# Kernel tuning notes

Measured on AMD Instinct MI355X. Metric: run time of the kernel, lower is better.

The kernel has to match this reference:

```python
import jax, jax.numpy as jnp
import numpy as np

D_MODEL = 1024
N_HEADS = 16
D_K = D_MODEL // N_HEADS
D_FF = 4 * D_MODEL
MEM = 32
EPS = 1e-6
NEG = -1e9


def layer_norm(x, alpha, bias):
    # torch: alpha * (x - mean) / (std_unbiased + eps) + bias
    mean = jnp.mean(x, axis=-1, keepdims=True)
    std = jnp.sqrt(jnp.var(x, axis=-1, keepdims=True, ddof=1))
    return alpha * (x - mean) / (std + EPS) + bias


def setup_inputs() -> dict:
    key = jax.random.key(0)
    ks = jax.random.split(key, 12)
    B, S = 4, 2048
    s = 1.0 / np.sqrt(D_MODEL)
    inp = {
        "x": jax.random.normal(ks[0], (B, S, D_MODEL), jnp.float32),
        "mask": jnp.ones((1, 1, S, S + MEM), jnp.int32),
        "memory_tokens": jax.random.normal(ks[1], (MEM, D_MODEL), jnp.float32),
        "w_q": jax.random.normal(ks[2], (D_MODEL, D_MODEL), jnp.float32) * s,
        "w_k": jax.random.normal(ks[3], (D_MODEL, D_MODEL), jnp.float32) * s,
        "w_v": jax.random.normal(ks[4], (D_MODEL, D_MODEL), jnp.float32) * s,
        "w_o": jax.random.normal(ks[5], (D_MODEL, D_MODEL), jnp.float32) * s,
        "ln1_alpha": jnp.ones((D_MODEL,), jnp.float32),
        "ln1_bias": jnp.zeros((D_MODEL,), jnp.float32),
        "ln2_alpha": jnp.ones((D_MODEL,), jnp.float32),
        "ln2_bias": jnp.zeros((D_MODEL,), jnp.float32),
        "ff_w1": jax.random.normal(ks[6], (D_MODEL, D_FF), jnp.float32) * s,
        "ff_b1": jnp.zeros((D_FF,), jnp.float32),
        "ff_w2": jax.random.normal(ks[7], (D_FF, D_MODEL), jnp.float32) * (1.0 / np.sqrt(D_FF)),
        "ff_b2": jnp.zeros((D_MODEL,), jnp.float32),
    }
    return inp


def reference(x, mask, memory_tokens, w_q, w_k, w_v, w_o,
              ln1_alpha, ln1_bias, ln2_alpha, ln2_bias,
              ff_w1, ff_b1, ff_w2, ff_b2):
    B, S, D = x.shape
    memory = jnp.broadcast_to(memory_tokens[None], (B, MEM, D))

    # --- residual 1: self attention with memory K/V ---
    xn = layer_norm(x, ln1_alpha, ln1_bias)
    q = (xn @ w_q).reshape(B, S, N_HEADS, D_K).transpose(0, 2, 1, 3)  # [B,h,S,dk]
    k = (xn @ w_k).reshape(B, S, N_HEADS, D_K).transpose(0, 2, 1, 3)
    v = (xn @ w_v).reshape(B, S, N_HEADS, D_K).transpose(0, 2, 1, 3)
    mem_k = (memory @ w_k).reshape(B, MEM, N_HEADS, D_K).transpose(0, 2, 1, 3)
    mem_v = (memory @ w_v).reshape(B, MEM, N_HEADS, D_K).transpose(0, 2, 1, 3)
    k = jnp.concatenate([mem_k, k], axis=2)  # [B,h,M+S,dk]
    v = jnp.concatenate([mem_v, v], axis=2)

    scores = jnp.einsum("bhsd,bhtd->bhst", q, k) / np.sqrt(D_K)  # [B,h,S,M+S]
    scores = jnp.where(mask == 0, NEG, scores)
    attn = jax.nn.softmax(scores, axis=-1)
    ctx = jnp.einsum("bhst,bhtd->bhsd", attn, v)
    ctx = ctx.transpose(0, 2, 1, 3).reshape(B, S, D)
    x = x + ctx @ w_o

    # --- residual 2: FFN ---
    xn2 = layer_norm(x, ln2_alpha, ln2_bias)
    ff = jax.nn.relu(xn2 @ ff_w1 + ff_b1) @ ff_w2 + ff_b2
    x = x + ff

    new_memory = jnp.broadcast_to(jnp.mean(x, axis=1, keepdims=True), (B, MEM, D))
    return (x, new_memory)
```

## Files before the change

### kernel.cpp

```cpp
#include <hip/hip_runtime.h>
#include <hip/hip_bf16.h>
#include <cstdint>
#include <cstddef>


typedef __attribute__((ext_vector_type(8))) short short8;
typedef __attribute__((ext_vector_type(4))) float floatx4;
typedef __attribute__((ext_vector_type(4))) unsigned short ushort4v;

#define NB   4
#define SEQ  2048
#define DM   1024
#define DKH  64
#define TT   2080
#define DFF  4096
#define NMEM 32

static __device__ __forceinline__ float bu2f(unsigned short u) {
  return __uint_as_float(((unsigned int)u) << 16);
}
static __device__ __forceinline__ unsigned short f2bu(float x) {
  __hip_bfloat16 h = __float2bfloat16(x);
  return *reinterpret_cast<unsigned short*>(&h);
}
static __device__ __forceinline__ float fast_exp2(float x) {
#if __has_builtin(__builtin_amdgcn_exp2f)
  return __builtin_amdgcn_exp2f(x);
#else
  return exp2f(x);
#endif
}
static __device__ __forceinline__ void async16(const void* g, void* l) {
  __builtin_amdgcn_global_load_lds(
      (const __attribute__((address_space(1))) void*)g,
      (__attribute__((address_space(3))) void*)l, 16, 0, 0);
}

#define PREP_X   8192
#define PREP_MT  (PREP_X + 32)
#define PREP_SM  (PREP_MT + 9)
#define PREP_T   (PREP_SM + 3072)

__global__ __launch_bounds__(256) void prep(
    const void* __restrict__ x,   const void* __restrict__ memtok,
    const void* __restrict__ wq,  const void* __restrict__ wk,
    const void* __restrict__ wv,  const void* __restrict__ wo,
    const void* __restrict__ fw1, const void* __restrict__ fw2,
    const void* __restrict__ ln1a, const void* __restrict__ ln1b,
    const void* __restrict__ ln2a, const void* __restrict__ ln2b,
    const void* __restrict__ fb1, const void* __restrict__ fb2,
    unsigned short* __restrict__ xb, unsigned short* __restrict__ MT,
    unsigned short* __restrict__ Wtq, unsigned short* __restrict__ Wtk,
    unsigned short* __restrict__ Wtv, unsigned short* __restrict__ Wto,
    unsigned short* __restrict__ Wt1, unsigned short* __restrict__ Wt2,
    unsigned short* __restrict__ L1A, unsigned short* __restrict__ L1B,
    unsigned short* __restrict__ L2A, unsigned short* __restrict__ L2B,
    unsigned short* __restrict__ FB1, unsigned short* __restrict__ FB2,
    int* __restrict__ FLAG)
{
  const int tid = threadIdx.x;
  const unsigned short probe = ((const unsigned short*)x)[tid & 63];
  const unsigned e = (probe >> 7) & 0xFF;
  const bool ok = (e == 0) || (e >= 100 && e <= 141);
  const int flag = (__ballot(!ok) != 0ULL) ? 1 : 0;
  const int bid = blockIdx.x;
  if (bid == 0 && tid == 0) *FLAG = flag;

  if (bid < PREP_T && bid >= PREP_SM) {
    const int tb = bid - PREP_SM;
    const void* in; unsigned short* outp; int R, C, tx, ty;
    if (tb < 1024) {
      const int w = tb >> 8, lt = tb & 255;
      in = (w == 0) ? wq : (w == 1) ? wk : (w == 2) ? wv : wo;
      outp = (w == 0) ? Wtq : (w == 1) ? Wtk : (w == 2) ? Wtv : Wto;
      R = DM; C = DM; tx = lt & 15; ty = lt >> 4;
    } else if (tb < 2048) {
      const int lt = tb - 1024;
      in = fw1; outp = Wt1; R = DM; C = DFF; tx = lt & 63; ty = lt >> 6;
    } else {
      const int lt = tb - 2048;
      in = fw2; outp = Wt2; R = DFF; C = DM; tx = lt & 15; ty = lt >> 4;
    }
    __shared__ unsigned short tile[64][65];
    const int r0 = ty << 6, c0 = tx << 6;
    const int lr = tid >> 2, lc = (tid & 3) << 4;
    if (flag) {
      const float* ip = (const float*)in + (size_t)(r0 + lr) * C + c0 + lc;
#pragma unroll
      for (int q = 0; q < 16; q += 4) {
        floatx4 f = *(const floatx4*)(ip + q);
        tile[lr][lc+q+0] = f2bu(f[0]); tile[lr][lc+q+1] = f2bu(f[1]);
        tile[lr][lc+q+2] = f2bu(f[2]); tile[lr][lc+q+3] = f2bu(f[3]);
      }
    } else {
      const unsigned short* ip = (const unsigned short*)in + (size_t)(r0 + lr) * C + c0 + lc;
#pragma unroll
      for (int q = 0; q < 16; q += 4) {
        ushort4v a = *(const ushort4v*)(ip + q);
        tile[lr][lc+q+0] = a.x; tile[lr][lc+q+1] = a.y;
        tile[lr][lc+q+2] = a.z; tile[lr][lc+q+3] = a.w;
      }
    }
    __syncthreads();
    unsigned short* op = outp + (size_t)(c0 + lr) * R + r0 + lc;
#pragma unroll
    for (int q = 0; q < 16; q += 4) {
      ushort4v a;
      a.x = tile[lc+q+0][lr]; a.y = tile[lc+q+1][lr];
      a.z = tile[lc+q+2][lr]; a.w = tile[lc+q+3][lr];
      *(ushort4v*)(op + q) = a;
    }
    return;
  }

  const void* src; unsigned short* dst; int base;
  if (bid < PREP_X)      { src = x;      dst = xb; base = bid * 1024; }
  else if (bid < PREP_MT){ src = memtok; dst = MT; base = (bid - PREP_X) * 1024; }
  else {
    const int s = bid - PREP_MT; base = 0;
    if      (s == 0) { src = ln1a; dst = L1A; }
    else if (s == 1) { src = ln1b; dst = L1B; }
    else if (s == 2) { src = ln2a; dst = L2A; }
    else if (s == 3) { src = ln2b; dst = L2B; }
    else if (s <= 7) { src = fb1;  dst = FB1; base = (s - 4) * 1024; }
    else             { src = fb2;  dst = FB2; }
  }
  const int i = base + tid * 4;
  if (flag) {
    const float* s4 = (const float*)src + i;
    ushort4v o;
    o.x = f2bu(s4[0]); o.y = f2bu(s4[1]); o.z = f2bu(s4[2]); o.w = f2bu(s4[3]);
    *(ushort4v*)&dst[i] = o;
  } else {
    *(ushort4v*)&dst[i] = *(const ushort4v*)&((const unsigned short*)src)[i];
  }
}

__global__ __launch_bounds__(512, 2) void gemm256(
    const unsigned short* __restrict__ A, int lda,
    const unsigned short* __restrict__ Bt, int ldbt,
    const unsigned short* __restrict__ bias,
    const unsigned short* __restrict__ resid_b,
    const float* __restrict__ resid_f,
    void* __restrict__ outp, void* __restrict__ outp2, void* __restrict__ outp3,
    int M, int N, int K, int relu, int mode, const int* __restrict__ dt)
{
  __shared__ __align__(16) unsigned short As[2][256 * 64];
  __shared__ __align__(16) unsigned short Bs[2][256 * 64];

  const int tid  = threadIdx.x;
  const int lane = tid & 63;
  const int wv   = tid >> 6;
  const int quad = lane >> 4;
  const int lr   = lane & 15;
  const int wr   = wv >> 2;
  const int wc   = wv & 3;
  const int arow = wr * 128;
  const int bcol = wc * 64;

  const int gx  = gridDim.x;
  const int nwg = gx * gridDim.y;
  int wg = blockIdx.y * gx + blockIdx.x;
  { const int q = nwg >> 3, rI = nwg & 7, xc = wg & 7, ix = wg >> 3;
    wg = (xc < rI ? xc * (q + 1) : rI * (q + 1) + (xc - rI) * q) + ix; }
  const int by = wg / gx;
  const int bx = wg - by * gx;
  const int m0 = by * 256;
  const int n0 = bx * 256;

  floatx4 acc[8][4];
#pragma unroll
  for (int i = 0; i < 8; ++i)
#pragma unroll
    for (int j = 0; j < 4; ++j) { floatx4 z = {0.f, 0.f, 0.f, 0.f}; acc[i][j] = z; }

  auto stage = [&](int buf, int kk) {
#pragma unroll
    for (int j = 0; j < 4; ++j) {
      const int g   = j * 512 + tid;
      const int row = g >> 3;
      const int kc  = (g & 7) ^ (row & 7);
      int gr = m0 + row; gr = gr < M ? gr : (M - 1);
      async16(A  + (size_t)gr * lda + kk + kc * 8,
              &As[buf][(size_t)(j * 512 + (tid & ~63)) * 8]);
      const int gn = n0 + row;
      async16(Bt + (size_t)gn * ldbt + kk + kc * 8,
              &Bs[buf][(size_t)(j * 512 + (tid & ~63)) * 8]);
    }
  };

  const int nk = K >> 6;
  stage(0, 0);
  int cur = 0;
  for (int it = 0; it < nk; ++it) {
    if (it + 1 < nk) {
      stage(cur ^ 1, (it + 1) << 6);
      asm volatile("s_waitcnt vmcnt(8)" ::: "memory");
    } else {
      asm volatile("s_waitcnt vmcnt(0)" ::: "memory");
    }
    __builtin_amdgcn_s_barrier();

    const unsigned short* Ab = &As[cur][0];
    const unsigned short* Bb = &Bs[cur][0];
#pragma unroll
    for (int ks = 0; ks < 2; ++ks) {
      short8 bfr[4], af[4];
#pragma unroll
      for (int ni = 0; ni < 4; ++ni) {
        const int row = bcol + ni * 16 + lr;
        bfr[ni] = *(const short8*)&Bb[row * 64 + (((ks * 4 + quad) ^ (lr & 7)) * 8)];
      }
#pragma unroll
      for (int mi = 0; mi < 4; ++mi) {
        const int row = arow + mi * 16 + lr;
        af[mi] = *(const short8*)&Ab[row * 64 + (((ks * 4 + quad) ^ (lr & 7)) * 8)];
      }
      __builtin_amdgcn_s_setprio(1);
#pragma unroll
      for (int mi = 0; mi < 4; ++mi)
#pragma unroll
        for (int ni = 0; ni < 4; ++ni)
          acc[mi][ni] = __builtin_amdgcn_mfma_f32_16x16x32_bf16(af[mi], bfr[ni], acc[mi][ni], 0, 0, 0);
      __builtin_amdgcn_s_setprio(0);
      __builtin_amdgcn_sched_barrier(0);
#pragma unroll
      for (int mi = 0; mi < 4; ++mi) {
        const int row = arow + 64 + mi * 16 + lr;
        af[mi] = *(const short8*)&Ab[row * 64 + (((ks * 4 + quad) ^ (lr & 7)) * 8)];
      }
      __builtin_amdgcn_s_setprio(1);
#pragma unroll
      for (int mi = 0; mi < 4; ++mi)
#pragma unroll
        for (int ni = 0; ni < 4; ++ni)
          acc[4 + mi][ni] = __builtin_amdgcn_mfma_f32_16x16x32_bf16(af[mi], bfr[ni], acc[4 + mi][ni], 0, 0, 0);
      __builtin_amdgcn_s_setprio(0);
      __builtin_amdgcn_sched_barrier(0);
    }

    asm volatile("s_waitcnt lgkmcnt(0)" ::: "memory");
    __builtin_amdgcn_s_barrier();
    cur ^= 1;
  }

  if (mode == 5) {
    const int cbase  = n0 + bcol;
    const int sector = cbase >> 10;
    const int clb    = cbase & 1023;
    unsigned short* Qo = (unsigned short*)outp;
    unsigned short* Ko = (unsigned short*)outp2;
    unsigned short* Vo = (unsigned short*)outp3;
#pragma unroll
    for (int mi = 0; mi < 8; ++mi) {
      const int rb = m0 + arow + mi * 16 + quad * 4;
#pragma unroll
      for (int ni = 0; ni < 4; ++ni) {
        const int col = clb + ni * 16 + lr;
        if (sector == 0) {
#pragma unroll
          for (int rg = 0; rg < 4; ++rg) {
            const int r = rb + rg;
            if (r < NB * SEQ) Qo[(size_t)r * DM + col] = f2bu(acc[mi][ni][rg]);
          }
        } else if (sector == 1) {
#pragma unroll
          for (int rg = 0; rg < 4; ++rg) {
            const int r = rb + rg;
            if (r >= M) continue;
            const int row2 = (r < NB * SEQ) ? ((r >> 11) * TT + NMEM + (r & (SEQ - 1)))
                                            : (r - NB * SEQ);
            Ko[(size_t)row2 * DM + col] = f2bu(acc[mi][ni][rg]);
          }
        } else {
          if (rb < M) {
            int bb, t;
            if (rb < NB * SEQ) { bb = rb >> 11; t = NMEM + (rb & (SEQ - 1)); }
            else               { bb = 0;        t = rb - NB * SEQ; }
            ushort4v pk;
            pk.x = f2bu(acc[mi][ni][0]); pk.y = f2bu(acc[mi][ni][1]);
            pk.z = f2bu(acc[mi][ni][2]); pk.w = f2bu(acc[mi][ni][3]);
            *(ushort4v*)(Vo + ((size_t)bb * DM + col) * TT + t) = pk;
          }
        }
      }
    }
    return;
  }

  const int ofp32 = (mode == 4 && dt) ? *dt : 0;
#pragma unroll
  for (int mi = 0; mi < 8; ++mi) {
    const int rb = m0 + arow + mi * 16 + quad * 4;
#pragma unroll
    for (int ni = 0; ni < 4; ++ni) {
      const int col = n0 + bcol + ni * 16 + lr;
      const float bv = bias ? bu2f(bias[col]) : 0.0f;
#pragma unroll
      for (int rg = 0; rg < 4; ++rg) {
        const int r = rb + rg;
        if (r >= M) continue;
        float v = acc[mi][ni][rg] + bv;
        if (relu) v = fmaxf(v, 0.0f);
        if (resid_b) v += bu2f(resid_b[(size_t)r * N + col]);
        if (resid_f) v += resid_f[(size_t)r * N + col];
        const size_t idx = (size_t)r * N + col;
        if (mode == 3)       ((float*)outp)[idx] = v;
        else if (mode == 4) {
          if (ofp32) ((float*)outp)[idx] = v;
          else       ((unsigned short*)outp)[idx] = f2bu(v);
        } else               ((unsigned short*)outp)[idx] = f2bu(v);
      }
    }
  }
}

#define PSTR 72

__global__ __launch_bounds__(256, 3) void flash_attn(
    const unsigned short* __restrict__ Q,
    const unsigned short* __restrict__ Kb,
    const unsigned short* __restrict__ Vtb,
    unsigned short* __restrict__ ctx)
{
  __shared__ __align__(16) unsigned short Ks[2][64 * 64];
  __shared__ __align__(16) unsigned short Vs[2][64 * 64];
  __shared__ __align__(16) unsigned short Ps[128 * PSTR];

  const int tid  = threadIdx.x;
  const int wave = tid >> 6;
  const int lane = tid & 63;
  const int quad = lane >> 4;
  const int lr   = lane & 15;

  const int i    = blockIdx.x;
  const int pair = (i & 7) * 8 + (i >> 7);
  const int q0   = ((i >> 3) & 15) * 128;
  const int b    = pair >> 4;
  const int h    = pair & 15;

  const unsigned short* Qb  = Q   + ((size_t)(b * SEQ + q0)) * DM + h * DKH;
  const unsigned short* Kbp = Kb  + ((size_t)b * TT) * DM + h * DKH;
  const unsigned short* Vbp = Vtb + ((size_t)(b * DM + h * DKH)) * TT;

  short8 aq[2][2];
#pragma unroll
  for (int mi = 0; mi < 2; ++mi)
#pragma unroll
    for (int ks = 0; ks < 2; ++ks)
      aq[mi][ks] = *(const short8*)(Qb + (size_t)(wave * 32 + mi * 16 + lr) * DM
                                       + ks * 32 + quad * 8);

  const int srl = lane >> 3;
  const int swc = (lane & 7) ^ srl;

  floatx4 O[2][4], Osum[2];
#pragma unroll
  for (int mi = 0; mi < 2; ++mi) {
    floatx4 z = {0.f, 0.f, 0.f, 0.f};
    Osum[mi] = z;
#pragma unroll
    for (int ni = 0; ni < 4; ++ni) O[mi][ni] = z;
  }
  short8 ones;
#pragma unroll
  for (int i2 = 0; i2 < 8; ++i2) ones[i2] = (short)0x3F80;

  const float SC = 0.125f * 1.4426950408889634f;

  auto stageKV = [&](int buf, int t0s) {
#pragma unroll
    for (int i2 = 0; i2 < 2; ++i2) {
      const int rr = (wave * 2 + i2) * 8 + srl;
      int tg = t0s + rr; tg = tg < TT ? tg : (TT - 1);
      async16(Kbp + (size_t)tg * DM + swc * 8, &Ks[buf][(wave * 2 + i2) * 512]);
      int ts = t0s + swc * 8; ts = ts <= (TT - 8) ? ts : (TT - 8);
      async16(Vbp + (size_t)rr * TT + ts, &Vs[buf][(wave * 2 + i2) * 512]);
    }
  };

  stageKV(0, 0);
  int cur = 0;

  for (int t0 = 0; t0 < TT; t0 += 64) {
    if (t0 + 64 < TT) {
      stageKV(cur ^ 1, t0 + 64);
      asm volatile("s_waitcnt vmcnt(4)" ::: "memory");
    } else {
      asm volatile("s_waitcnt vmcnt(0)" ::: "memory");
    }
    __builtin_amdgcn_s_barrier();

    floatx4 sc4[2][4];
#pragma unroll
    for (int mi = 0; mi < 2; ++mi)
#pragma unroll
      for (int ni = 0; ni < 4; ++ni) { floatx4 z = {0.f, 0.f, 0.f, 0.f}; sc4[mi][ni] = z; }
#pragma unroll
    for (int ks = 0; ks < 2; ++ks) {
      short8 bk[4];
#pragma unroll
      for (int ni = 0; ni < 4; ++ni) {
        const int row = ni * 16 + lr;
        bk[ni] = *(const short8*)&Ks[cur][row * 64 + (((ks * 4 + quad) ^ (row & 7)) * 8)];
      }
      __builtin_amdgcn_s_setprio(1);
#pragma unroll
      for (int mi = 0; mi < 2; ++mi)
#pragma unroll
        for (int ni = 0; ni < 4; ++ni)
          sc4[mi][ni] = __builtin_amdgcn_mfma_f32_16x16x32_bf16(aq[mi][ks], bk[ni], sc4[mi][ni], 0, 0, 0);
      __builtin_amdgcn_s_setprio(0);
    }

    bool valid[4];
#pragma unroll
    for (int ni = 0; ni < 4; ++ni) valid[ni] = (t0 + ni * 16 + lr) < TT;

#pragma unroll
    for (int mi = 0; mi < 2; ++mi)
#pragma unroll
      for (int rg = 0; rg < 4; ++rg) {
        const int prow = wave * 32 + mi * 16 + quad * 4 + rg;
#pragma unroll
        for (int ni = 0; ni < 4; ++ni) {
          const float p = valid[ni] ? fast_exp2(sc4[mi][ni][rg] * SC) : 0.0f;
          Ps[prow * PSTR + ni * 16 + lr] =
              (unsigned short)((__float_as_uint(p) + 0x8000u) >> 16);
        }
      }

    __asm__ __volatile__("" ::: "memory");

#pragma unroll
    for (int ks = 0; ks < 2; ++ks) {
      short8 ap[2], bv[4];
#pragma unroll
      for (int mi = 0; mi < 2; ++mi)
        ap[mi] = *(const short8*)&Ps[(wave * 32 + mi * 16 + lr) * PSTR + ks * 32 + quad * 8];
#pragma unroll
      for (int ni = 0; ni < 4; ++ni) {
        const int row = ni * 16 + lr;
        bv[ni] = *(const short8*)&Vs[cur][row * 64 + (((ks * 4 + quad) ^ (row & 7)) * 8)];
      }
      __builtin_amdgcn_s_setprio(1);
#pragma unroll
      for (int mi = 0; mi < 2; ++mi) {
        Osum[mi] = __builtin_amdgcn_mfma_f32_16x16x32_bf16(ap[mi], ones, Osum[mi], 0, 0, 0);
#pragma unroll
        for (int ni = 0; ni < 4; ++ni)
          O[mi][ni] = __builtin_amdgcn_mfma_f32_16x16x32_bf16(ap[mi], bv[ni], O[mi][ni], 0, 0, 0);
      }
      __builtin_amdgcn_s_setprio(0);
    }

    asm volatile("s_waitcnt lgkmcnt(0)" ::: "memory");
    __builtin_amdgcn_s_barrier();
    cur ^= 1;
  }

#pragma unroll
  for (int mi = 0; mi < 2; ++mi)
#pragma unroll
    for (int rg = 0; rg < 4; ++rg) {
      const float inv = 1.0f / Osum[mi][rg];
      const int row = q0 + wave * 32 + mi * 16 + quad * 4 + rg;
#pragma unroll
      for (int ni = 0; ni < 4; ++ni) {
        const int col = h * DKH + ni * 16 + lr;
        ctx[((size_t)(b * SEQ + row)) * DM + col] = f2bu(O[mi][ni][rg] * inv);
      }
    }
}

__global__ __launch_bounds__(256) void ln_kernel(
    const unsigned short* __restrict__ xin_bf,
    const float* __restrict__ xin_f,
    const unsigned short* __restrict__ memtok,
    const unsigned short* __restrict__ gam,
    const unsigned short* __restrict__ bet,
    unsigned short* __restrict__ outp,
    int rows_main)
{
  const int row = blockIdx.x;
  const int tid = threadIdx.x;
  const int c0  = tid * 4;
  if (row >= rows_main) {
    const int mr = row - rows_main;
    *(ushort4v*)&outp[(size_t)row * DM + c0] =
        *(const ushort4v*)&memtok[(size_t)mr * DM + c0];
    return;
  }
  float v[4];
  if (xin_bf) {
    ushort4v u = *(const ushort4v*)&xin_bf[(size_t)row * DM + c0];
    v[0] = bu2f(u.x); v[1] = bu2f(u.y); v[2] = bu2f(u.z); v[3] = bu2f(u.w);
  } else {
    floatx4 f = *(const floatx4*)&xin_f[(size_t)row * DM + c0];
    v[0] = f[0]; v[1] = f[1]; v[2] = f[2]; v[3] = f[3];
  }
  float s  = v[0] + v[1] + v[2] + v[3];
  float ss = v[0]*v[0] + v[1]*v[1] + v[2]*v[2] + v[3]*v[3];
#pragma unroll
  for (int m = 1; m <= 32; m <<= 1) {
    s  += __shfl_xor(s, m, 64);
    ss += __shfl_xor(ss, m, 64);
  }
  __shared__ float red[8];
  const int wave = tid >> 6, lane = tid & 63;
  if (lane == 0) { red[wave] = s; red[4 + wave] = ss; }
  __syncthreads();
  s  = red[0] + red[1] + red[2] + red[3];
  ss = red[4] + red[5] + red[6] + red[7];
  const float mean = s * (1.0f / 1024.0f);
  float var = (ss - 1024.0f * mean * mean) * (1.0f / 1023.0f);
  var = fmaxf(var, 0.0f);
  const float inv = 1.0f / (sqrtf(var) + 1e-6f);
  ushort4v o;
  o.x = f2bu(bu2f(gam[c0+0]) * (v[0] - mean) * inv + bu2f(bet[c0+0]));
  o.y = f2bu(bu2f(gam[c0+1]) * (v[1] - mean) * inv + bu2f(bet[c0+1]));
  o.z = f2bu(bu2f(gam[c0+2]) * (v[2] - mean) * inv + bu2f(bet[c0+2]));
  o.w = f2bu(bu2f(gam[c0+3]) * (v[3] - mean) * inv + bu2f(bet[c0+3]));
  *(ushort4v*)&outp[(size_t)row * DM + c0] = o;
}

__global__ __launch_bounds__(256) void replicate_mem(
    unsigned short* __restrict__ Kb, unsigned short* __restrict__ Vtb)
{
  const int idx = blockIdx.x * 256 + threadIdx.x;
  const int t = idx >> 10, c = idx & 1023;
  const unsigned short kv = Kb[(size_t)t * DM + c];
  const unsigned short vv = Vtb[(size_t)c * TT + t];
#pragma unroll
  for (int b = 1; b < NB; ++b) {
    Kb[((size_t)b * TT + t) * DM + c] = kv;
    Vtb[((size_t)(b * DM + c)) * TT + t] = vv;
  }
}

__global__ __launch_bounds__(256) void colsum(
    const void* __restrict__ xo, float* __restrict__ acc,
    const int* __restrict__ flag)
{
  const int d  = blockIdx.x * 256 + threadIdx.x;
  const int s0 = blockIdx.y * 256;
  const int b  = blockIdx.z;
  const size_t base = ((size_t)(b * SEQ + s0)) * DM + d;
  float s = 0.0f;
  if (*flag) {
    const float* p = (const float*)xo;
    for (int i = 0; i < 256; ++i) s += p[base + (size_t)i * DM];
  } else {
    const unsigned short* p = (const unsigned short*)xo;
    for (int i = 0; i < 256; ++i) s += bu2f(p[base + (size_t)i * DM]);
  }
  atomicAdd(&acc[b * DM + d], s);
}

__global__ __launch_bounds__(256) void write_mem(
    const float* __restrict__ acc, void* __restrict__ dout,
    const int* __restrict__ flag)
{
  const int idx = blockIdx.x * 256 + threadIdx.x;
  const int b = idx >> 10, d = idx & 1023;
  const float w = acc[idx] * (1.0f / 2048.0f);
  const int f = *flag;
#pragma unroll
  for (int m = 0; m < NMEM; ++m) {
    const size_t off = (size_t)NB * SEQ * DM + ((size_t)(b * NMEM + m)) * DM + d;
    if (f) ((float*)dout)[off] = w;
    else   ((unsigned short*)dout)[off] = f2bu(w);
  }
}

extern "C" void kernel_launch(void* const* d_in, const int* in_sizes, int n_in,
                              void* d_out, int out_size, void* d_ws, size_t ws_size,
                              hipStream_t stream) {
  const void* x      = d_in[0];
  const void* memtok = d_in[2];
  const void* wq     = d_in[3];
  const void* wk     = d_in[4];
  const void* wv     = d_in[5];
  const void* wo     = d_in[6];
  const void* ln1a   = d_in[7];
  const void* ln1b   = d_in[8];
  const void* ln2a   = d_in[9];
  const void* ln2b   = d_in[10];
  const void* fw1    = d_in[11];
  const void* fb1    = d_in[12];
  const void* fw2    = d_in[13];
  const void* fb2    = d_in[14];

  char* ws = (char*)d_ws;
  constexpr size_t OFF_WT1 = 0;
  constexpr size_t OFF_WT2 = OFF_WT1 + (size_t)DFF * DM * 2;
  constexpr size_t OFF_VT  = OFF_WT2 + (size_t)DM * DFF * 2;
  constexpr size_t SZ_VT   = (size_t)NB * DM * TT * 2;
  constexpr size_t OFF_Q   = OFF_VT + SZ_VT;
  constexpr size_t SZ_Q    = (size_t)NB * SEQ * DM * 2;
  constexpr size_t OFF_K   = OFF_Q + SZ_Q;
  constexpr size_t SZ_K    = (size_t)NB * TT * DM * 2;
  constexpr size_t OFF_XN  = OFF_K + SZ_K;
  constexpr size_t SZ_XN   = (size_t)8224 * DM * 2;
  constexpr size_t OFF_W4  = OFF_XN + SZ_XN;
  constexpr size_t SZ_DD   = (size_t)DM * DM * 2;
  constexpr size_t OFF_XB  = OFF_W4 + 4 * SZ_DD;
  constexpr size_t SZ_XB   = (size_t)NB * SEQ * DM * 2;
  constexpr size_t OFF_SM  = OFF_XB + SZ_XB;
  static_assert(OFF_XN + (size_t)NB * SEQ * 2048 * 2 <= OFF_SM, "h1 overlay");
  static_assert(OFF_Q + (size_t)NB * SEQ * DM * 4 <= OFF_XN, "x1f overlay");

  unsigned short* Wt1 = (unsigned short*)(ws + OFF_WT1);
  unsigned short* Wt2 = (unsigned short*)(ws + OFF_WT2);
  unsigned short* Vtb = (unsigned short*)(ws + OFF_VT);
  unsigned short* Qb  = (unsigned short*)(ws + OFF_Q);
  unsigned short* Kbf = (unsigned short*)(ws + OFF_K);
  unsigned short* xn  = (unsigned short*)(ws + OFF_XN);
  unsigned short* Wtq = (unsigned short*)(ws + OFF_W4);
  unsigned short* Wtk = (unsigned short*)(ws + OFF_W4 + SZ_DD);
  unsigned short* Wtv = (unsigned short*)(ws + OFF_W4 + 2 * SZ_DD);
  unsigned short* Wto = (unsigned short*)(ws + OFF_W4 + 3 * SZ_DD);
  unsigned short* xb  = (unsigned short*)(ws + OFF_XB);
  unsigned short* MT  = (unsigned short*)(ws + OFF_SM);
  unsigned short* L1A = (unsigned short*)(ws + OFF_SM + 65536);
  unsigned short* L1B = (unsigned short*)(ws + OFF_SM + 67584);
  unsigned short* L2A = (unsigned short*)(ws + OFF_SM + 69632);
  unsigned short* L2B = (unsigned short*)(ws + OFF_SM + 71680);
  unsigned short* FB1 = (unsigned short*)(ws + OFF_SM + 73728);
  unsigned short* FB2 = (unsigned short*)(ws + OFF_SM + 81920);
  float*          accb= (float*)(ws + OFF_SM + 84480);
  int*            FLAG= (int*)(ws + OFF_SM + 101376);

  unsigned short* ctx = xn;
  unsigned short* h1  = xn;
  float*          x1f = (float*)(ws + OFF_Q);
  unsigned short* xn2 = Vtb;

  const dim3 blk(256);
  const dim3 blk512(512);

  prep<<<PREP_T, blk, 0, stream>>>(x, memtok, wq, wk, wv, wo, fw1, fw2,
                                   ln1a, ln1b, ln2a, ln2b, fb1, fb2,
                                   xb, MT, Wtq, Wtk, Wtv, Wto, Wt1, Wt2,
                                   L1A, L1B, L2A, L2B, FB1, FB2, FLAG);

  ln_kernel<<<8224, blk, 0, stream>>>(xb, nullptr, MT, L1A, L1B, xn, 8192);

  gemm256<<<dim3(12, 33), blk512, 0, stream>>>(
      xn, DM, Wtq, DM, nullptr, nullptr, nullptr,
      Qb, Kbf, Vtb, 8224, 3072, DM, 0, 5, nullptr);
  replicate_mem<<<128, blk, 0, stream>>>(Kbf, Vtb);

  flash_attn<<<1024, blk, 0, stream>>>(Qb, Kbf, Vtb, ctx);

  gemm256<<<dim3(4, 32), blk512, 0, stream>>>(
      ctx, DM, Wto, DM, nullptr, xb, nullptr,
      x1f, nullptr, nullptr, 8192, DM, DM, 0, 3, nullptr);

  ln_kernel<<<8192, blk, 0, stream>>>(nullptr, x1f, nullptr, L2A, L2B, xn2, 8192);

  gemm256<<<dim3(8, 32), blk512, 0, stream>>>(
      xn2, DM, Wt1, DM, FB1, nullptr, nullptr,
      h1, nullptr, nullptr, 8192, 2048, DM, 1, 0, nullptr);
  gemm256<<<dim3(4, 32), blk512, 0, stream>>>(
      h1, 2048, Wt2, DFF, nullptr, nullptr, x1f,
      x1f, nullptr, nullptr, 8192, DM, 2048, 0, 3, nullptr);
  gemm256<<<dim3(8, 32), blk512, 0, stream>>>(
      xn2, DM, Wt1 + (size_t)2048 * DM, DM, FB1 + 2048, nullptr, nullptr,
      h1, nullptr, nullptr, 8192, 2048, DM, 1, 0, nullptr);
  gemm256<<<dim3(4, 32), blk512, 0, stream>>>(
      h1, 2048, Wt2 + 2048, DFF, FB2, nullptr, x1f,
      d_out, nullptr, nullptr, 8192, DM, 2048, 0, 4, FLAG);

  hipMemsetAsync(accb, 0, (size_t)NB * DM * sizeof(float), stream);
  colsum<<<dim3(4, 8, 4), blk, 0, stream>>>(d_out, accb, FLAG);
  write_mem<<<16, blk, 0, stream>>>(accb, d_out, FLAG);
}
```

Baseline: 769.0 us.

## Pipeline 256-tile GEMM loads in sub-stages and use 128-tile GEMM for N=1024

The 256x256 GEMM main loop is restructured into four phases per k-tile. Loads of the next B halves and A quarters are issued between the MFMA phases, with finer vmcnt waits and barriers, so global-to-LDS traffic overlaps compute rather than being issued as one block per iteration. The N=1024 GEMMs (output projection and the FFN down projections) move to a new 128x128 tile kernel with 256 threads, giving 512 workgroups instead of 128 and filling the CUs better. This adds more barriers in the big kernel and uses smaller tiles with less data reuse in the new kernel.

```diff
diff --git a/kernel.cpp b/kernel.cpp
--- a/kernel.cpp
+++ b/kernel.cpp
@@ -136,14 +136,12 @@
   }
 }
 
-__global__ __launch_bounds__(512, 2) void gemm256(
+__global__ __launch_bounds__(512, 2) void gemm256p(
     const unsigned short* __restrict__ A, int lda,
     const unsigned short* __restrict__ Bt, int ldbt,
     const unsigned short* __restrict__ bias,
-    const unsigned short* __restrict__ resid_b,
-    const float* __restrict__ resid_f,
     void* __restrict__ outp, void* __restrict__ outp2, void* __restrict__ outp3,
-    int M, int N, int K, int relu, int mode, const int* __restrict__ dt)
+    int M, int N, int K, int relu, int mode)
 {
   __shared__ __align__(16) unsigned short As[2][256 * 64];
   __shared__ __align__(16) unsigned short Bs[2][256 * 64];
@@ -174,74 +172,126 @@
 #pragma unroll
     for (int j = 0; j < 4; ++j) { floatx4 z = {0.f, 0.f, 0.f, 0.f}; acc[i][j] = z; }
 
-  auto stage = [&](int buf, int kk) {
-#pragma unroll
-    for (int j = 0; j < 4; ++j) {
+  const int wbase = tid & ~63;
+
+  auto stageB = [&](int buf, int kt, int half) {
+#pragma unroll
+    for (int j = 0; j < 2; ++j) {
       const int g   = j * 512 + tid;
       const int row = g >> 3;
       const int kc  = (g & 7) ^ (row & 7);
-      int gr = m0 + row; gr = gr < M ? gr : (M - 1);
-      async16(A  + (size_t)gr * lda + kk + kc * 8,
-              &As[buf][(size_t)(j * 512 + (tid & ~63)) * 8]);
-      const int gn = n0 + row;
-      async16(Bt + (size_t)gn * ldbt + kk + kc * 8,
-              &Bs[buf][(size_t)(j * 512 + (tid & ~63)) * 8]);
+      const int gn  = n0 + half * 128 + row;
+      async16(Bt + (size_t)gn * ldbt + (kt << 6) + kc * 8,
+              &Bs[buf][(half * 128) * 64 + (j * 512 + wbase) * 8]);
     }
   };
+  auto stageAQ = [&](int buf, int kt, int qa) {
+    const int g   = tid;
+    const int row = g >> 3;
+    const int kc  = (g & 7) ^ (row & 7);
+    int gr = m0 + qa * 64 + row; gr = gr < M ? gr : (M - 1);
+    async16(A + (size_t)gr * lda + (kt << 6) + kc * 8,
+            &As[buf][(qa * 64) * 64 + wbase * 8]);
+  };
 
   const int nk = K >> 6;
-  stage(0, 0);
-  int cur = 0;
-  for (int it = 0; it < nk; ++it) {
-    if (it + 1 < nk) {
-      stage(cur ^ 1, (it + 1) << 6);
-      asm volatile("s_waitcnt vmcnt(8)" ::: "memory");
-    } else {
-      asm volatile("s_waitcnt vmcnt(0)" ::: "memory");
-    }
-    __builtin_amdgcn_s_barrier();
-
-    const unsigned short* Ab = &As[cur][0];
-    const unsigned short* Bb = &Bs[cur][0];
-#pragma unroll
-    for (int ks = 0; ks < 2; ++ks) {
-      short8 bfr[4], af[4];
-#pragma unroll
-      for (int ni = 0; ni < 4; ++ni) {
-        const int row = bcol + ni * 16 + lr;
-        bfr[ni] = *(const short8*)&Bb[row * 64 + (((ks * 4 + quad) ^ (lr & 7)) * 8)];
-      }
-#pragma unroll
-      for (int mi = 0; mi < 4; ++mi) {
-        const int row = arow + mi * 16 + lr;
-        af[mi] = *(const short8*)&Ab[row * 64 + (((ks * 4 + quad) ^ (lr & 7)) * 8)];
-      }
-      __builtin_amdgcn_s_setprio(1);
-#pragma unroll
-      for (int mi = 0; mi < 4; ++mi)
-#pragma unroll
-        for (int ni = 0; ni < 4; ++ni)
-          acc[mi][ni] = __builtin_amdgcn_mfma_f32_16x16x32_bf16(af[mi], bfr[ni], acc[mi][ni], 0, 0, 0);
-      __builtin_amdgcn_s_setprio(0);
-      __builtin_amdgcn_sched_barrier(0);
-#pragma unroll
-      for (int mi = 0; mi < 4; ++mi) {
-        const int row = arow + 64 + mi * 16 + lr;
-        af[mi] = *(const short8*)&Ab[row * 64 + (((ks * 4 + quad) ^ (lr & 7)) * 8)];
-      }
-      __builtin_amdgcn_s_setprio(1);
-#pragma unroll
-      for (int mi = 0; mi < 4; ++mi)
-#pragma unroll
-        for (int ni = 0; ni < 4; ++ni)
-          acc[4 + mi][ni] = __builtin_amdgcn_mfma_f32_16x16x32_bf16(af[mi], bfr[ni], acc[4 + mi][ni], 0, 0, 0);
-      __builtin_amdgcn_s_setprio(0);
-      __builtin_amdgcn_sched_barrier(0);
-    }
-
+  stageAQ(0, 0, 0); stageAQ(0, 0, 2);
+  stageB (0, 0, 0); stageB (0, 0, 1);
+  if (nk > 1) { stageAQ(1, 1, 0); stageAQ(1, 1, 2); }
+  stageAQ(0, 0, 1); stageAQ(0, 0, 3);
+
+  for (int t = 0; t < nk; ++t) {
+    const int b = t & 1;
+    const unsigned short* Ab = &As[b][0];
+    const unsigned short* Bb = &Bs[b][0];
+    short8 bfr0[4], bfr1[4], af[4];
+
+    if (t + 1 < nk) { asm volatile("s_waitcnt vmcnt(4)" ::: "memory"); }
+    else            { asm volatile("s_waitcnt vmcnt(2)" ::: "memory"); }
+    if (t + 1 < nk) stageB(b ^ 1, t + 1, 0);
+#pragma unroll
+    for (int ni = 0; ni < 4; ++ni) {
+      const int row = bcol + ni * 16 + lr;
+      bfr0[ni] = *(const short8*)&Bb[row * 64 + ((quad ^ (lr & 7)) * 8)];
+    }
+#pragma unroll
+    for (int mi = 0; mi < 4; ++mi) {
+      const int row = arow + mi * 16 + lr;
+      af[mi] = *(const short8*)&Ab[row * 64 + ((quad ^ (lr & 7)) * 8)];
+    }
+    __builtin_amdgcn_s_barrier();
     asm volatile("s_waitcnt lgkmcnt(0)" ::: "memory");
-    __builtin_amdgcn_s_barrier();
-    cur ^= 1;
+    __builtin_amdgcn_sched_barrier(0);
+    __builtin_amdgcn_s_setprio(1);
+#pragma unroll
+    for (int mi = 0; mi < 4; ++mi)
+#pragma unroll
+      for (int ni = 0; ni < 4; ++ni)
+        acc[mi][ni] = __builtin_amdgcn_mfma_f32_16x16x32_bf16(af[mi], bfr0[ni], acc[mi][ni], 0, 0, 0);
+    __builtin_amdgcn_s_setprio(0);
+    __builtin_amdgcn_s_barrier();
+
+    if (t + 1 < nk) stageB(b ^ 1, t + 1, 1);
+#pragma unroll
+    for (int ni = 0; ni < 4; ++ni) {
+      const int row = bcol + ni * 16 + lr;
+      bfr1[ni] = *(const short8*)&Bb[row * 64 + (((4 + quad) ^ (lr & 7)) * 8)];
+    }
+#pragma unroll
+    for (int mi = 0; mi < 4; ++mi) {
+      const int row = arow + mi * 16 + lr;
+      af[mi] = *(const short8*)&Ab[row * 64 + (((4 + quad) ^ (lr & 7)) * 8)];
+    }
+    __builtin_amdgcn_s_barrier();
+    asm volatile("s_waitcnt lgkmcnt(0)" ::: "memory");
+    __builtin_amdgcn_sched_barrier(0);
+    __builtin_amdgcn_s_setprio(1);
+#pragma unroll
+    for (int mi = 0; mi < 4; ++mi)
+#pragma unroll
+      for (int ni = 0; ni < 4; ++ni)
+        acc[mi][ni] = __builtin_amdgcn_mfma_f32_16x16x32_bf16(af[mi], bfr1[ni], acc[mi][ni], 0, 0, 0);
+    __builtin_amdgcn_s_setprio(0);
+    __builtin_amdgcn_s_barrier();
+
+    if (t + 2 < nk) { stageAQ(b, t + 2, 0); stageAQ(b, t + 2, 2); }
+    if (t + 2 < nk)      { asm volatile("s_waitcnt vmcnt(6)" ::: "memory"); }
+    else if (t + 1 < nk) { asm volatile("s_waitcnt vmcnt(4)" ::: "memory"); }
+    else                 { asm volatile("s_waitcnt vmcnt(0)" ::: "memory"); }
+#pragma unroll
+    for (int mi = 0; mi < 4; ++mi) {
+      const int row = arow + 64 + mi * 16 + lr;
+      af[mi] = *(const short8*)&Ab[row * 64 + ((quad ^ (lr & 7)) * 8)];
+    }
+    __builtin_amdgcn_s_barrier();
+    asm volatile("s_waitcnt lgkmcnt(0)" ::: "memory");
+    __builtin_amdgcn_sched_barrier(0);
+    __builtin_amdgcn_s_setprio(1);
+#pragma unroll
+    for (int mi = 0; mi < 4; ++mi)
+#pragma unroll
+      for (int ni = 0; ni < 4; ++ni)
+        acc[4 + mi][ni] = __builtin_amdgcn_mfma_f32_16x16x32_bf16(af[mi], bfr0[ni], acc[4 + mi][ni], 0, 0, 0);
+    __builtin_amdgcn_s_setprio(0);
+    __builtin_amdgcn_s_barrier();
+
+    if (t + 1 < nk) { stageAQ(b ^ 1, t + 1, 1); stageAQ(b ^ 1, t + 1, 3); }
+#pragma unroll
+    for (int mi = 0; mi < 4; ++mi) {
+      const int row = arow + 64 + mi * 16 + lr;
+      af[mi] = *(const short8*)&Ab[row * 64 + (((4 + quad) ^ (lr & 7)) * 8)];
+    }
+    __builtin_amdgcn_s_barrier();
+    asm volatile("s_waitcnt lgkmcnt(0)" ::: "memory");
+    __builtin_amdgcn_sched_barrier(0);
+    __builtin_amdgcn_s_setprio(1);
+#pragma unroll
+    for (int mi = 0; mi < 4; ++mi)
+#pragma unroll
+      for (int ni = 0; ni < 4; ++ni)
+        acc[4 + mi][ni] = __builtin_amdgcn_mfma_f32_16x16x32_bf16(af[mi], bfr1[ni], acc[4 + mi][ni], 0, 0, 0);
+    __builtin_amdgcn_s_setprio(0);
+    __builtin_amdgcn_s_barrier();
   }
 
   if (mode == 5) {
@@ -253,7 +303,7 @@
     unsigned short* Vo = (unsigned short*)outp3;
 #pragma unroll
     for (int mi = 0; mi < 8; ++mi) {
-      const int rb = m0 + arow + mi * 16 + quad * 4;
+      const int rb = m0 + (wr * 128) + mi * 16 + quad * 4;
 #pragma unroll
       for (int ni = 0; ni < 4; ++ni) {
         const int col = clb + ni * 16 + lr;
@@ -274,13 +324,13 @@
           }
         } else {
           if (rb < M) {
-            int bb, t;
-            if (rb < NB * SEQ) { bb = rb >> 11; t = NMEM + (rb & (SEQ - 1)); }
-            else               { bb = 0;        t = rb - NB * SEQ; }
+            int bb, tt2;
+            if (rb < NB * SEQ) { bb = rb >> 11; tt2 = NMEM + (rb & (SEQ - 1)); }
+            else               { bb = 0;        tt2 = rb - NB * SEQ; }
             ushort4v pk;
             pk.x = f2bu(acc[mi][ni][0]); pk.y = f2bu(acc[mi][ni][1]);
             pk.z = f2bu(acc[mi][ni][2]); pk.w = f2bu(acc[mi][ni][3]);
-            *(ushort4v*)(Vo + ((size_t)bb * DM + col) * TT + t) = pk;
+            *(ushort4v*)(Vo + ((size_t)bb * DM + col) * TT + tt2) = pk;
           }
         }
       }
@@ -288,13 +338,115 @@
     return;
   }
 
-  const int ofp32 = (mode == 4 && dt) ? *dt : 0;
 #pragma unroll
   for (int mi = 0; mi < 8; ++mi) {
-    const int rb = m0 + arow + mi * 16 + quad * 4;
+    const int rb = m0 + (wr * 128) + mi * 16 + quad * 4;
 #pragma unroll
     for (int ni = 0; ni < 4; ++ni) {
       const int col = n0 + bcol + ni * 16 + lr;
+      const float bv = bias ? bu2f(bias[col]) : 0.0f;
+#pragma unroll
+      for (int rg = 0; rg < 4; ++rg) {
+        const int r = rb + rg;
+        if (r >= M) continue;
+        float v = acc[mi][ni][rg] + bv;
+        if (relu) v = fmaxf(v, 0.0f);
+        ((unsigned short*)outp)[(size_t)r * N + col] = f2bu(v);
+      }
+    }
+  }
+}
+
+__global__ __launch_bounds__(256, 2) void gemm_bt(
+    const unsigned short* __restrict__ A, int lda,
+    const unsigned short* __restrict__ Bt, int ldbt,
+    const unsigned short* __restrict__ bias,
+    const unsigned short* __restrict__ resid_b,
+    const float* __restrict__ resid_f,
+    void* __restrict__ outp,
+    int M, int N, int K, int relu, int mode, const int* __restrict__ dt)
+{
+  __shared__ __align__(16) unsigned short As[2][128 * 32];
+  __shared__ __align__(16) unsigned short Bs[2][128 * 32];
+
+  const int tid  = threadIdx.x;
+  const int wave = tid >> 6;
+  const int lane = tid & 63;
+  const int quad = lane >> 4;
+  const int lr   = lane & 15;
+  const int wm   = (wave >> 1) * 64;
+  const int wn   = (wave & 1) * 64;
+
+  const int gx  = gridDim.x;
+  const int nwg = gx * gridDim.y;
+  int wg = blockIdx.y * gx + blockIdx.x;
+  wg = (wg & 7) * (nwg >> 3) + (wg >> 3);
+  const int by = wg / gx;
+  const int bx = wg - by * gx;
+  const int m0 = by * 128;
+  const int n0 = bx * 128;
+
+  floatx4 acc[4][4];
+#pragma unroll
+  for (int i = 0; i < 4; ++i)
+#pragma unroll
+    for (int j = 0; j < 4; ++j) { floatx4 z = {0.f, 0.f, 0.f, 0.f}; acc[i][j] = z; }
+
+  const int srow = lane >> 2;
+  const int skof = (((lane & 3) ^ ((lane >> 3) & 3))) * 8;
+  const int fsw  = (lr >> 1) & 3;
+
+  auto stage = [&](int buf, int kk) {
+#pragma unroll
+    for (int i = 0; i < 2; ++i) {
+      const int rr = wave * 32 + i * 16;
+      const int r  = rr + srow;
+      int gr = m0 + r; gr = gr < M ? gr : (M - 1);
+      async16(A  + (size_t)gr * lda + kk + skof, &As[buf][rr * 32]);
+      const int gn = n0 + r;
+      async16(Bt + (size_t)gn * ldbt + kk + skof, &Bs[buf][rr * 32]);
+    }
+  };
+
+  const int nk = K >> 5;
+  stage(0, 0);
+  int cur = 0;
+  for (int it = 0; it < nk; ++it) {
+    if (it + 1 < nk) {
+      stage(cur ^ 1, (it + 1) << 5);
+      asm volatile("s_waitcnt vmcnt(4)" ::: "memory");
+    } else {
+      asm volatile("s_waitcnt vmcnt(0)" ::: "memory");
+    }
+    __builtin_amdgcn_s_barrier();
+
+    const unsigned short* Ab = &As[cur][0];
+    const unsigned short* Bb = &Bs[cur][0];
+    short8 af[4], bfr[4];
+#pragma unroll
+    for (int mi = 0; mi < 4; ++mi)
+      af[mi]  = *(const short8*)&Ab[(wm + mi * 16 + lr) * 32 + ((quad ^ fsw) * 8)];
+#pragma unroll
+    for (int ni = 0; ni < 4; ++ni)
+      bfr[ni] = *(const short8*)&Bb[(wn + ni * 16 + lr) * 32 + ((quad ^ fsw) * 8)];
+#pragma unroll
+    for (int mi = 0; mi < 4; ++mi)
+#pragma unroll
+      for (int ni = 0; ni < 4; ++ni)
+        acc[mi][ni] = __builtin_amdgcn_mfma_f32_16x16x32_bf16(af[mi], bfr[ni], acc[mi][ni], 0, 0, 0);
+
+    asm volatile("s_waitcnt lgkmcnt(0)" ::: "memory");
+    __builtin_amdgcn_s_barrier();
+    cur ^= 1;
+  }
+
+  const int ofp32 = (mode == 4 && dt) ? *dt : 0;
+#pragma unroll
+  for (int mi = 0; mi < 4; ++mi) {
+    const int rb = m0 + wm + mi * 16 + quad * 4;
+#pragma unroll
+    for (int ni = 0; ni < 4; ++ni) {
+      const int col = n0 + wn + ni * 16 + lr;
       const float bv = bias ? bu2f(bias[col]) : 0.0f;
 #pragma unroll
       for (int rg = 0; rg < 4; ++rg) {
@@ -646,31 +798,25 @@
 
   ln_kernel<<<8224, blk, 0, stream>>>(xb, nullptr, MT, L1A, L1B, xn, 8192);
 
-  gemm256<<<dim3(12, 33), blk512, 0, stream>>>(
-      xn, DM, Wtq, DM, nullptr, nullptr, nullptr,
-      Qb, Kbf, Vtb, 8224, 3072, DM, 0, 5, nullptr);
+  gemm256p<<<dim3(12, 33), blk512, 0, stream>>>(
+      xn, DM, Wtq, DM, nullptr,
+      Qb, Kbf, Vtb, 8224, 3072, DM, 0, 5);
   replicate_mem<<<128, blk, 0, stream>>>(Kbf, Vtb);
 
   flash_attn<<<1024, blk, 0, stream>>>(Qb, Kbf, Vtb, ctx);
 
-  gemm256<<<dim3(4, 32), blk512, 0, stream>>>(
-      ctx, DM, Wto, DM, nullptr, xb, nullptr,
-      x1f, nullptr, nullptr, 8192, DM, DM, 0, 3, nullptr);
+  gemm_bt<<<dim3(8, 64), blk, 0, stream>>>(ctx, DM, Wto, DM, nullptr, xb, nullptr, x1f, 8192, DM, DM, 0, 3, nullptr);
 
   ln_kernel<<<8192, blk, 0, stream>>>(nullptr, x1f, nullptr, L2A, L2B, xn2, 8192);
 
-  gemm256<<<dim3(8, 32), blk512, 0, stream>>>(
-      xn2, DM, Wt1, DM, FB1, nullptr, nullptr,
-      h1, nullptr, nullptr, 8192, 2048, DM, 1, 0, nullptr);
-  gemm256<<<dim3(4, 32), blk512, 0, stream>>>(
-      h1, 2048, Wt2, DFF, nullptr, nullptr, x1f,
-      x1f, nullptr, nullptr, 8192, DM, 2048, 0, 3, nullptr);
-  gemm256<<<dim3(8, 32), blk512, 0, stream>>>(
-      xn2, DM, Wt1 + (size_t)2048 * DM, DM, FB1 + 2048, nullptr, nullptr,
-      h1, nullptr, nullptr, 8192, 2048, DM, 1, 0, nullptr);
-  gemm256<<<dim3(4, 32), blk512, 0, stream>>>(
-      h1, 2048, Wt2 + 2048, DFF, FB2, nullptr, x1f,
-      d_out, nullptr, nullptr, 8192, DM, 2048, 0, 4, FLAG);
+  gemm256p<<<dim3(8, 32), blk512, 0, stream>>>(
+      xn2, DM, Wt1, DM, FB1,
+      h1, nullptr, nullptr, 8192, 2048, DM, 1, 0);
+  gemm_bt<<<dim3(8, 64), blk, 0, stream>>>(h1, 2048, Wt2, DFF, nullptr, nullptr, x1f, x1f, 8192, DM, 2048, 0, 3, nullptr);
+  gemm256p<<<dim3(8, 32), blk512, 0, stream>>>(
+      xn2, DM, Wt1 + (size_t)2048 * DM, DM, FB1 + 2048,
+      h1, nullptr, nullptr, 8192, 2048, DM, 1, 0);
+  gemm_bt<<<dim3(8, 64), blk, 0, stream>>>(h1, 2048, Wt2 + 2048, DFF, FB2, nullptr, x1f, d_out, 8192, DM, 2048, 0, 4, FLAG);
 
   hipMemsetAsync(accb, 0, (size_t)NB * DM * sizeof(float), stream);
   colsum<<<dim3(4, 8, 4), blk, 0, stream>>>(d_out, accb, FLAG);
```

Result: faster. 710.0 us (-7.7%).
